# Kernel tuning notes

Hardware: AMD Instinct MI355X
Metric: run time of the kernel (lower is better)

The kernel has to match this reference:

```python
import jax, jax.numpy as jnp
import numpy as np

LN_EPS = 1e-5

def setup_inputs() -> dict:
    key = jax.random.key(0)
    k1, k2, k3 = jax.random.split(key, 3)
    L, B, D = 2048, 8, 1024
    x = jax.random.normal(k1, (L, B, D), dtype=jnp.float32)
    c = jnp.zeros((B, D), dtype=jnp.float32)
    W = jax.random.normal(k2, (D, 3 * D), dtype=jnp.float32) * 0.02
    # bias init from _init_bias: u-bias 0, f-bias 0.5, r-bias 0
    b = jnp.concatenate([jnp.zeros(D), jnp.full((D,), 0.5), jnp.zeros(D)]).astype(jnp.float32)
    gamma = jnp.ones((D,), dtype=jnp.float32)
    beta = jnp.zeros((D,), dtype=jnp.float32)
    return {"x": x, "c": c, "W": W, "b": b, "gamma": gamma, "beta": beta}

def reference(x, c, W, b, gamma, beta):
    # LayerNorm over last dim
    mu = jnp.mean(x, axis=-1, keepdims=True)
    var = jnp.mean(jnp.square(x - mu), axis=-1, keepdims=True)
    x_norm = (x - mu) * jax.lax.rsqrt(var + LN_EPS) * gamma + beta
    # Fused u/f/r projection: [L,B,3D]
    ufr = jnp.einsum('lbd,de->lbe', x_norm, W) + b
    u, f, r = jnp.split(ufr, 3, axis=-1)
    f_gate = jax.nn.sigmoid(f)
    r_gate = jax.nn.sigmoid(r)
    # Linear recurrence c_t = f_t * c_{t-1} + (1-f_t) * u_t via scan over time
    def step(c_prev, fu):
        f_t, u_t = fu
        c_t = f_t * c_prev + (1.0 - f_t) * u_t
        return c_t, c_t
    last_c, c_stack = jax.lax.scan(step, c, (f_gate, u))
    hs = r_gate * jnp.tanh(c_stack) + (1.0 - r_gate) * x_norm
    return x + hs, last_c
```

## Files before the change

### kernel.cpp

```cpp
#include <hip/hip_runtime.h>
#include <hip/hip_bf16.h>
#include <hip/hip_fp8.h>


typedef unsigned short u16;
typedef unsigned char u8;
typedef __bf16 bf16x8 __attribute__((ext_vector_type(8)));
typedef float f32x4 __attribute__((ext_vector_type(4)));

#define L_DIM 2048
#define B_DIM 8
#define D_DIM 1024
#define M_DIM (L_DIM * B_DIM)
#define K_DIM D_DIM
#define N_DIM (3 * D_DIM)
#define NCH 32
#define CLEN (L_DIM / NCH)
#define NT (K_DIM / 64)

#define LDS_B 65536
#define LDS_DUMMY 131072
#define LDS_TOTAL 147456
#define L8_B 32768
#define L8_DUMMY 65536
#define L8_TOTAL 73728

__device__ __forceinline__ float bf2f(u16 h) {
    unsigned int u = ((unsigned int)h) << 16;
    float f;
    __builtin_memcpy(&f, &u, 4);
    return f;
}

__device__ __forceinline__ u16 f2bf(float f) {
    unsigned int u;
    __builtin_memcpy(&u, &f, 4);
    u = u + 0x7fff + ((u >> 16) & 1);
    return (u16)(u >> 16);
}

__device__ __forceinline__ u8 f2e4(float v) {
    __hip_fp8_e4m3 t(v);
    return (u8)t.__x;
}

__device__ __forceinline__ void async16(void* lds, const void* g) {
    __builtin_amdgcn_global_load_lds(
        (const __attribute__((address_space(1))) void*)g,
        (__attribute__((address_space(3))) void*)lds, 16, 0, 0);
}

__global__ __launch_bounds__(256) void ln_kernel(const float* __restrict__ x,
                                                 const float* __restrict__ gamma,
                                                 const float* __restrict__ beta,
                                                 u16* __restrict__ xn,
                                                 u8* __restrict__ xq,
                                                 float2* __restrict__ mrs) {
    int row = blockIdx.x;
    int tid = threadIdx.x;
    const float4* xr = (const float4*)(x + (size_t)row * D_DIM);
    float4 v = xr[tid];
    float s = v.x + v.y + v.z + v.w;
    float q = v.x * v.x + v.y * v.y + v.z * v.z + v.w * v.w;
    #pragma unroll
    for (int off = 32; off; off >>= 1) {
        s += __shfl_down(s, off);
        q += __shfl_down(q, off);
    }
    __shared__ float ss[4], qq[4];
    int lane = tid & 63, wv = tid >> 6;
    if (lane == 0) { ss[wv] = s; qq[wv] = q; }
    __syncthreads();
    s = ss[0] + ss[1] + ss[2] + ss[3];
    q = qq[0] + qq[1] + qq[2] + qq[3];
    float mu = s * (1.0f / D_DIM);
    float var = q * (1.0f / D_DIM) - mu * mu;
    float rs = rsqrtf(var + 1e-5f);
    if (tid == 0) mrs[row] = make_float2(mu, rs);
    float4 g = ((const float4*)gamma)[tid];
    float4 bt = ((const float4*)beta)[tid];
    float n0 = (v.x - mu) * rs * g.x + bt.x;
    float n1 = (v.y - mu) * rs * g.y + bt.y;
    float n2 = (v.z - mu) * rs * g.z + bt.z;
    float n3 = (v.w - mu) * rs * g.w + bt.w;
    ushort4 o;
    o.x = f2bf(n0); o.y = f2bf(n1); o.z = f2bf(n2); o.w = f2bf(n3);
    ((ushort4*)(xn + (size_t)row * D_DIM))[tid] = o;
    uchar4 o8;
    o8.x = f2e4(n0); o8.y = f2e4(n1); o8.z = f2e4(n2); o8.w = f2e4(n3);
    ((uchar4*)(xq + (size_t)row * D_DIM))[tid] = o8;
}

__global__ __launch_bounds__(256) void wt_kernel(const float* __restrict__ W,
                                                 u16* __restrict__ Wt,
                                                 u8* __restrict__ Wf8) {
    __shared__ float t[64][65];
    int k0 = blockIdx.x * 64;
    int n0 = blockIdx.y * 64;
    int col = threadIdx.x & 63;
    int rg4 = threadIdx.x >> 6;
    #pragma unroll
    for (int j = 0; j < 16; ++j) {
        int r = rg4 * 16 + j;
        t[r][col] = W[(size_t)(k0 + r) * N_DIM + n0 + col];
    }
    __syncthreads();
    if (n0 < 1024) {
        #pragma unroll
        for (int j = 0; j < 16; ++j) {
            int nr = rg4 * 16 + j;
            Wt[(size_t)(n0 + nr) * K_DIM + k0 + col] = f2bf(t[col][nr]);
        }
    } else {
        #pragma unroll
        for (int j = 0; j < 16; ++j) {
            int nr = rg4 * 16 + j;
            Wf8[(size_t)(n0 - 1024 + nr) * K_DIM + k0 + col] = f2e4(t[col][nr] * 64.0f);
        }
    }
}

__global__ __launch_bounds__(512, 2) void gemm_kernel(const u16* __restrict__ A,
                                                      const u16* __restrict__ Bt,
                                                      const float* __restrict__ bias,
                                                      u16* __restrict__ uo) {
    extern __shared__ char lds[];
    const int tid = threadIdx.x;
    const int wave = tid >> 6, lane = tid & 63;
    const int lm = lane & 15, lg = lane >> 4;
    const int wm = wave >> 2, wn = wave & 3;
    const int m0 = blockIdx.x * 256;
    const int n0 = blockIdx.y * 256;

    const int xk0 = ((0 | lg) ^ (lm & 7)) << 4;
    const int xk1 = ((4 | lg) ^ (lm & 7)) << 4;
    const char* pA0 = lds + (wm * 128 + lm) * 128 + xk0;
    const char* pA1 = lds + (wm * 128 + lm) * 128 + xk1;
    const char* pB0 = lds + LDS_B + (wn * 64 + lm) * 128 + xk0;
    const char* pB1 = lds + LDS_B + (wn * 64 + lm) * 128 + xk1;

    const int c1 = 512 + tid;
    const int r0 = tid >> 3, cc0 = (tid & 7) ^ (r0 & 7);
    const int r1 = c1 >> 3, cc1 = (c1 & 7) ^ (r1 & 7);
    const char* gA0 = (const char*)A + ((size_t)(m0 + r0) * K_DIM + cc0 * 8) * 2;
    const char* gA1 = (const char*)A + ((size_t)(m0 + r1) * K_DIM + cc1 * 8) * 2;
    const char* gB0 = (const char*)Bt + ((size_t)(n0 + r0) * K_DIM + cc0 * 8) * 2;
    const char* gB1 = (const char*)Bt + ((size_t)(n0 + r1) * K_DIM + cc1 * 8) * 2;
    char* dstW = lds + wave * 1024;

    f32x4 acc[8][4] = {};
    bf16x8 av[4], aw[4], bv0[4], bv1[4];

    auto stageA = [&](int t1, int h) {
        char* dst = (t1 < NT) ? (dstW + ((t1 & 1) << 15) + (h << 14))
                              : (lds + LDS_DUMMY + wave * 1024);
        int ko = ((t1 & 15) << 7) + (h << 18);
        async16(dst,        gA0 + ko);
        async16(dst + 8192, gA1 + ko);
    };
    auto stageB = [&](int t2, int h) {
        char* dst = (t2 < NT) ? (dstW + LDS_B + ((t2 & 1) << 15) + (h << 14))
                              : (lds + LDS_DUMMY + wave * 1024);
        int ko = ((t2 & 15) << 7) + (h << 18);
        async16(dst,        gB0 + ko);
        async16(dst + 8192, gB1 + ko);
    };

#define LDA(dst, pbase, bb, mf0)                                                \
    do { _Pragma("unroll")                                                      \
        for (int q = 0; q < 4; ++q)                                             \
            dst[q] = *(const bf16x8*)(pbase + (bb) * 32768 + ((mf0) + q) * 2048); \
    } while (0)

#define LDB(dst, pbase, bb)                                                     \
    do { _Pragma("unroll")                                                      \
        for (int nf = 0; nf < 4; ++nf)                                          \
            dst[nf] = *(const bf16x8*)(pbase + (bb) * 32768 + nf * 2048);       \
    } while (0)

#define MFMA16(r0q, afr, bfr)                                                   \
    do { _Pragma("unroll")                                                      \
        for (int q = 0; q < 4; ++q)                                             \
            _Pragma("unroll")                                                   \
            for (int nf = 0; nf < 4; ++nf)                                      \
                acc[(r0q) + q][nf] = __builtin_amdgcn_mfma_f32_16x16x32_bf16(   \
                    afr[q], bfr[nf], acc[(r0q) + q][nf], 0, 0, 0);              \
    } while (0)

#define PH_SYNC()                                                               \
    do { __builtin_amdgcn_s_barrier();                                          \
         asm volatile("s_waitcnt lgkmcnt(0)");                                  \
         __builtin_amdgcn_sched_barrier(0); } while (0)

#define TILE_BODY(t, bb)                                                        \
    do {                                                                        \
        LDA(av, pA0, bb, 0);                                                    \
        LDB(bv0, pB0, bb);                                                      \
        stageA((t) + 1, 0);                                                     \
        PH_SYNC();                                                              \
        __builtin_amdgcn_s_setprio(1);  MFMA16(0, av, bv0);                     \
        __builtin_amdgcn_s_setprio(0);  __builtin_amdgcn_s_barrier();           \
        LDA(av, pA1, bb, 0);                                                    \
        LDB(bv1, pB1, bb);                                                      \
        stageA((t) + 1, 1);                                                     \
        PH_SYNC();                                                              \
        __builtin_amdgcn_s_setprio(1);  MFMA16(0, av, bv1);                     \
        __builtin_amdgcn_s_setprio(0);  __builtin_amdgcn_s_barrier();           \
        LDA(aw, pA0, bb, 4);                                                    \
        stageB((t) + 2, 0);                                                     \
        PH_SYNC();                                                              \
        __builtin_amdgcn_s_setprio(1);  MFMA16(4, aw, bv0);                     \
        __builtin_amdgcn_s_setprio(0);  __builtin_amdgcn_s_barrier();           \
        LDA(aw, pA1, bb, 4);                                                    \
        stageB((t) + 2, 1);                                                     \
        PH_SYNC();                                                              \
        __builtin_amdgcn_s_setprio(1);  MFMA16(4, aw, bv1);                     \
        __builtin_amdgcn_s_setprio(0);                                          \
        asm volatile("s_waitcnt vmcnt(4)" ::: "memory");                        \
        __builtin_amdgcn_s_barrier();                                           \
    } while (0)

    stageA(0, 0); stageA(0, 1);
    stageB(0, 0); stageB(0, 1);
    stageB(1, 0); stageB(1, 1);
    asm volatile("s_waitcnt vmcnt(4)" ::: "memory");
    __builtin_amdgcn_s_barrier();

    for (int t = 0; t < NT; t += 2) {
        TILE_BODY(t, 0);
        TILE_BODY(t + 1, 1);
    }

    float bb4[4];
    #pragma unroll
    for (int nf = 0; nf < 4; ++nf) bb4[nf] = bias[n0 + wn * 64 + nf * 16 + lm];
    const int cmb = n0 + wn * 64 + lm;
    #pragma unroll
    for (int mf = 0; mf < 8; ++mf) {
        #pragma unroll
        for (int j = 0; j < 4; ++j) {
            int row = m0 + wm * 128 + mf * 16 + lg * 4 + j;
            u16* rp = uo + (size_t)row * D_DIM + cmb;
            #pragma unroll
            for (int nf = 0; nf < 4; ++nf)
                rp[nf * 16] = f2bf(acc[mf][nf][j] + bb4[nf]);
        }
    }
#undef LDA
#undef LDB
#undef MFMA16
#undef PH_SYNC
#undef TILE_BODY
}

__global__ __launch_bounds__(512, 2) void gemm8_kernel(const u8* __restrict__ A8,
                                                       const u8* __restrict__ B8,
                                                       const float* __restrict__ bias,
                                                       u16* __restrict__ fo,
                                                       u16* __restrict__ ro) {
    extern __shared__ char lds[];
    const int tid = threadIdx.x;
    const int wave = tid >> 6, lane = tid & 63;
    const int lm = lane & 15, lg = lane >> 4;
    const int wm = wave >> 2, wn = wave & 3;
    const int m0 = blockIdx.x * 256;
    const int n0 = blockIdx.y * 256;

    const int sl = (lg & 1) * 8;
    const int xq0 = (((0 + (lg >> 1)) ^ (lm & 3)) << 4) + sl;
    const int xq1 = (((2 + (lg >> 1)) ^ (lm & 3)) << 4) + sl;
    const char* pA0 = lds + (wm * 128 + lm) * 64 + xq0;
    const char* pA1 = lds + (wm * 128 + lm) * 64 + xq1;
    const char* pB0 = lds + L8_B + (wn * 64 + lm) * 64 + xq0;
    const char* pB1 = lds + L8_B + (wn * 64 + lm) * 64 + xq1;

    const int r0 = tid >> 2, cq0 = (tid & 3) ^ (r0 & 3);
    const char* gA = (const char*)A8 + (size_t)(m0 + r0) * K_DIM + cq0 * 16;
    const char* gB = (const char*)B8 + (size_t)(n0 + r0) * K_DIM + cq0 * 16;
    char* dstW = lds + wave * 1024;

    f32x4 acc[8][4] = {};
    long av[4], aw[4], bv0[4], bv1[4];

    auto stageA = [&](int t1, int h) {
        char* dst = (t1 < NT) ? (dstW + ((t1 & 1) << 14) + (h << 13))
                              : (lds + L8_DUMMY + wave * 1024);
        async16(dst, gA + ((t1 & 15) << 6) + (h << 17));
    };
    auto stageB = [&](int t2, int h) {
        char* dst = (t2 < NT) ? (dstW + L8_B + ((t2 & 1) << 14) + (h << 13))
                              : (lds + L8_DUMMY + wave * 1024);
        async16(dst, gB + ((t2 & 15) << 6) + (h << 17));
    };

#define LDA8(dst, pbase, bb, mf0)                                               \
    do { _Pragma("unroll")                                                      \
        for (int q = 0; q < 4; ++q)                                             \
            dst[q] = *(const long*)(pbase + (bb) * 16384 + ((mf0) + q) * 1024); \
    } while (0)

#define LDB8(dst, pbase, bb)                                                    \
    do { _Pragma("unroll")                                                      \
        for (int nf = 0; nf < 4; ++nf)                                          \
            dst[nf] = *(const long*)(pbase + (bb) * 16384 + nf * 1024);         \
    } while (0)

#define MFMA16F8(r0q, afr, bfr)                                                 \
    do { _Pragma("unroll")                                                      \
        for (int q = 0; q < 4; ++q)                                             \
            _Pragma("unroll")                                                   \
            for (int nf = 0; nf < 4; ++nf)                                      \
                acc[(r0q) + q][nf] = __builtin_amdgcn_mfma_f32_16x16x32_fp8_fp8(\
                    afr[q], bfr[nf], acc[(r0q) + q][nf], 0, 0, 0);              \
    } while (0)

#define PH_SYNC()                                                               \
    do { __builtin_amdgcn_s_barrier();                                          \
         asm volatile("s_waitcnt lgkmcnt(0)");                                  \
         __builtin_amdgcn_sched_barrier(0); } while (0)

#define TILE_BODY8(t, bb)                                                       \
    do {                                                                        \
        LDA8(av, pA0, bb, 0);                                                   \
        LDB8(bv0, pB0, bb);                                                     \
        stageA((t) + 1, 0);                                                     \
        PH_SYNC();                                                              \
        __builtin_amdgcn_s_setprio(1);  MFMA16F8(0, av, bv0);                   \
        __builtin_amdgcn_s_setprio(0);  __builtin_amdgcn_s_barrier();           \
        LDA8(av, pA1, bb, 0);                                                   \
        LDB8(bv1, pB1, bb);                                                     \
        stageA((t) + 1, 1);                                                     \
        PH_SYNC();                                                              \
        __builtin_amdgcn_s_setprio(1);  MFMA16F8(0, av, bv1);                   \
        __builtin_amdgcn_s_setprio(0);  __builtin_amdgcn_s_barrier();           \
        LDA8(aw, pA0, bb, 4);                                                   \
        stageB((t) + 2, 0);                                                     \
        PH_SYNC();                                                              \
        __builtin_amdgcn_s_setprio(1);  MFMA16F8(4, aw, bv0);                   \
        __builtin_amdgcn_s_setprio(0);  __builtin_amdgcn_s_barrier();           \
        LDA8(aw, pA1, bb, 4);                                                   \
        stageB((t) + 2, 1);                                                     \
        PH_SYNC();                                                              \
        __builtin_amdgcn_s_setprio(1);  MFMA16F8(4, aw, bv1);                   \
        __builtin_amdgcn_s_setprio(0);                                          \
        asm volatile("s_waitcnt vmcnt(2)" ::: "memory");                        \
        __builtin_amdgcn_s_barrier();                                           \
    } while (0)

    stageA(0, 0); stageA(0, 1);
    stageB(0, 0); stageB(0, 1);
    stageB(1, 0); stageB(1, 1);
    asm volatile("s_waitcnt vmcnt(2)" ::: "memory");
    __builtin_amdgcn_s_barrier();

    for (int t = 0; t < NT; t += 2) {
        TILE_BODY8(t, 0);
        TILE_BODY8(t + 1, 1);
    }

    int seg = n0 >> 10;
    u16* outp = seg ? ro : fo;
    float bb4[4];
    #pragma unroll
    for (int nf = 0; nf < 4; ++nf) bb4[nf] = bias[1024 + n0 + wn * 64 + nf * 16 + lm];
    const int cmb = (n0 + wn * 64 + lm) & 1023;
    #pragma unroll
    for (int mf = 0; mf < 8; ++mf) {
        #pragma unroll
        for (int j = 0; j < 4; ++j) {
            int row = m0 + wm * 128 + mf * 16 + lg * 4 + j;
            u16* rp = outp + (size_t)row * D_DIM + cmb;
            #pragma unroll
            for (int nf = 0; nf < 4; ++nf) {
                float val = acc[mf][nf][j] * 0.015625f + bb4[nf];
                rp[nf * 16] = f2bf(1.0f / (1.0f + __expf(-val)));
            }
        }
    }
#undef LDA8
#undef LDB8
#undef MFMA16F8
#undef PH_SYNC
#undef TILE_BODY8
}

__global__ __launch_bounds__(256) void scan1_kernel(const u16* __restrict__ fg,
                                                    const u16* __restrict__ u,
                                                    float* __restrict__ Aa,
                                                    float* __restrict__ Ss) {
    int ch = blockIdx.x;
    int bd = (blockIdx.y * 256 + threadIdx.x) * 2;
    int b = bd >> 10, d = bd & 1023;
    float a0 = 1.0f, a1 = 1.0f, s0 = 0.0f, s1 = 0.0f;
    for (int t = ch * CLEN; t < ch * CLEN + CLEN; ++t) {
        size_t idx = ((size_t)(t * B_DIM + b) << 10) + d;
        ushort2 f2 = *(const ushort2*)(fg + idx);
        ushort2 u2 = *(const ushort2*)(u + idx);
        float f0 = bf2f(f2.x), f1 = bf2f(f2.y);
        float v0 = bf2f(u2.x), v1 = bf2f(u2.y);
        s0 = f0 * s0 + (1.0f - f0) * v0;
        s1 = f1 * s1 + (1.0f - f1) * v1;
        a0 *= f0;
        a1 *= f1;
    }
    int o = ch * 8192 + bd;
    *(float2*)(Aa + o) = make_float2(a0, a1);
    *(float2*)(Ss + o) = make_float2(s0, s1);
}

__global__ __launch_bounds__(256) void scan2_kernel(const float* __restrict__ Aa,
                                                    const float* __restrict__ Ss,
                                                    const float* __restrict__ c0,
                                                    float* __restrict__ cs,
                                                    float* __restrict__ lastc) {
    int bd = blockIdx.x * 256 + threadIdx.x;
    float c = c0[bd];
    #pragma unroll 4
    for (int ch = 0; ch < NCH; ++ch) {
        cs[ch * 8192 + bd] = c;
        c = Aa[ch * 8192 + bd] * c + Ss[ch * 8192 + bd];
    }
    lastc[bd] = c;
}

__global__ __launch_bounds__(256) void scan3_kernel(const float* __restrict__ cs,
                                                    const u16* __restrict__ fg,
                                                    const u16* __restrict__ u,
                                                    const u16* __restrict__ rg,
                                                    const float2* __restrict__ mrs,
                                                    const float* __restrict__ gamma,
                                                    const float* __restrict__ beta,
                                                    const float* __restrict__ x,
                                                    float* __restrict__ out) {
    int ch = blockIdx.x;
    int bd = (blockIdx.y * 256 + threadIdx.x) * 2;
    int b = bd >> 10, d = bd & 1023;
    float2 gm = *(const float2*)(gamma + d);
    float2 bt = *(const float2*)(beta + d);
    float c0v = cs[ch * 8192 + bd];
    float c1v = cs[ch * 8192 + bd + 1];
    for (int t = ch * CLEN; t < ch * CLEN + CLEN; ++t) {
        size_t idx = ((size_t)(t * B_DIM + b) << 10) + d;
        ushort2 f2 = *(const ushort2*)(fg + idx);
        ushort2 u2 = *(const ushort2*)(u + idx);
        ushort2 r2 = *(const ushort2*)(rg + idx);
        float2 x2 = *(const float2*)(x + idx);
        float2 mr = mrs[t * B_DIM + b];
        float f0 = bf2f(f2.x), f1 = bf2f(f2.y);
        float v0 = bf2f(u2.x), v1 = bf2f(u2.y);
        float r0 = bf2f(r2.x), r1 = bf2f(r2.y);
        float n0 = (x2.x - mr.x) * mr.y * gm.x + bt.x;
        float n1 = (x2.y - mr.x) * mr.y * gm.y + bt.y;
        c0v = f0 * c0v + (1.0f - f0) * v0;
        c1v = f1 * c1v + (1.0f - f1) * v1;
        float h0 = r0 * tanhf(c0v) + (1.0f - r0) * n0;
        float h1 = r1 * tanhf(c1v) + (1.0f - r1) * n1;
        *(float2*)(out + idx) = make_float2(x2.x + h0, x2.y + h1);
    }
}

extern "C" void kernel_launch(void* const* d_in, const int* in_sizes, int n_in,
                              void* d_out, int out_size, void* d_ws, size_t ws_size,
                              hipStream_t stream) {
    const float* x     = (const float*)d_in[0];
    const float* c0    = (const float*)d_in[1];
    const float* W     = (const float*)d_in[2];
    const float* b     = (const float*)d_in[3];
    const float* gamma = (const float*)d_in[4];
    const float* beta  = (const float*)d_in[5];
    float* out = (float*)d_out;
    float* lastc = out + (size_t)M_DIM * D_DIM;
    u8* xq = (u8*)d_out;

    char* w = (char*)d_ws;
    u16* xn = (u16*)w;  w += (size_t)M_DIM * D_DIM * 2;
    u16* Wt = (u16*)w;  w += (size_t)N_DIM * K_DIM * 2;
    u16* ug = (u16*)w;  w += (size_t)M_DIM * D_DIM * 2;
    u16* fg = (u16*)w;  w += (size_t)M_DIM * D_DIM * 2;
    u16* rg = (u16*)w;  w += (size_t)M_DIM * D_DIM * 2;
    float* Aa = (float*)w; w += (size_t)NCH * 8192 * 4;
    float* Ss = (float*)w; w += (size_t)NCH * 8192 * 4;
    float* cs = (float*)w; w += (size_t)NCH * 8192 * 4;
    float2* mrs = (float2*)w; w += (size_t)M_DIM * 8;
    u8* Wf8 = (u8*)w; w += (size_t)2048 * K_DIM;

    hipFuncSetAttribute(reinterpret_cast<const void*>(gemm_kernel),
                        hipFuncAttributeMaxDynamicSharedMemorySize, LDS_TOTAL);
    hipFuncSetAttribute(reinterpret_cast<const void*>(gemm8_kernel),
                        hipFuncAttributeMaxDynamicSharedMemorySize, L8_TOTAL);

    ln_kernel<<<M_DIM, 256, 0, stream>>>(x, gamma, beta, xn, xq, mrs);
    wt_kernel<<<dim3(K_DIM / 64, N_DIM / 64), 256, 0, stream>>>(W, Wt, Wf8);
    gemm_kernel<<<dim3(M_DIM / 256, 4), 512, LDS_TOTAL, stream>>>(xn, Wt, b, ug);
    gemm8_kernel<<<dim3(M_DIM / 256, 8), 512, L8_TOTAL, stream>>>(xq, Wf8, b, fg, rg);
    scan1_kernel<<<dim3(NCH, 16), 256, 0, stream>>>(fg, ug, Aa, Ss);
    scan2_kernel<<<32, 256, 0, stream>>>(Aa, Ss, c0, cs, lastc);
    scan3_kernel<<<dim3(NCH, 16), 256, 0, stream>>>(cs, fg, ug, rg, mrs, gamma, beta, x, out);
}
```

Measured before the change: 214.5 us.

## Double FP8 GEMM K-tile depth to 128 with wider LDS swizzle

The FP8 gate GEMM now stages 128-byte K slices per tile instead of 64, halving the number of main-loop iterations and barriers. The LDS layout grows to 128-byte rows with an 8-way XOR swizzle, and each thread issues two async 16-byte loads per stage. Wait counts and the four-phase tile body are adjusted so every A fragment is reused across more B fragments. LDS use rises from 72KB to 144KB, which likely drops occupancy from two blocks per CU to one.

```diff
diff --git a/kernel.cpp b/kernel.cpp
--- a/kernel.cpp
+++ b/kernel.cpp
@@ -17,13 +17,11 @@
 #define NCH 32
 #define CLEN (L_DIM / NCH)
 #define NT (K_DIM / 64)
+#define NT8 (K_DIM / 128)
 
 #define LDS_B 65536
 #define LDS_DUMMY 131072
 #define LDS_TOTAL 147456
-#define L8_B 32768
-#define L8_DUMMY 65536
-#define L8_TOTAL 73728
 
 __device__ __forceinline__ float bf2f(u16 h) {
     unsigned int u = ((unsigned int)h) << 16;
@@ -266,52 +264,60 @@
     const int m0 = blockIdx.x * 256;
     const int n0 = blockIdx.y * 256;
 
-    const int sl = (lg & 1) * 8;
-    const int xq0 = (((0 + (lg >> 1)) ^ (lm & 3)) << 4) + sl;
-    const int xq1 = (((2 + (lg >> 1)) ^ (lm & 3)) << 4) + sl;
-    const char* pA0 = lds + (wm * 128 + lm) * 64 + xq0;
-    const char* pA1 = lds + (wm * 128 + lm) * 64 + xq1;
-    const char* pB0 = lds + L8_B + (wn * 64 + lm) * 64 + xq0;
-    const char* pB1 = lds + L8_B + (wn * 64 + lm) * 64 + xq1;
-
-    const int r0 = tid >> 2, cq0 = (tid & 3) ^ (r0 & 3);
-    const char* gA = (const char*)A8 + (size_t)(m0 + r0) * K_DIM + cq0 * 16;
-    const char* gB = (const char*)B8 + (size_t)(n0 + r0) * K_DIM + cq0 * 16;
+    const int lgb = (lg & 1) * 8, lg2 = lg >> 1;
+    const int xq0 = (((0 + lg2) ^ (lm & 7)) << 4) + lgb;
+    const int xq1 = (((2 + lg2) ^ (lm & 7)) << 4) + lgb;
+    const int xq2 = (((4 + lg2) ^ (lm & 7)) << 4) + lgb;
+    const int xq3 = (((6 + lg2) ^ (lm & 7)) << 4) + lgb;
+    const char* pA = lds + (wm * 128 + lm) * 128;
+    const char* pB = lds + LDS_B + (wn * 64 + lm) * 128;
+
+    const int c1 = 512 + tid;
+    const int r0 = tid >> 3, cc0 = (tid & 7) ^ (r0 & 7);
+    const int r1 = c1 >> 3, cc1 = (c1 & 7) ^ (r1 & 7);
+    const char* gA0 = (const char*)A8 + (size_t)(m0 + r0) * K_DIM + cc0 * 16;
+    const char* gA1 = (const char*)A8 + (size_t)(m0 + r1) * K_DIM + cc1 * 16;
+    const char* gB0 = (const char*)B8 + (size_t)(n0 + r0) * K_DIM + cc0 * 16;
+    const char* gB1 = (const char*)B8 + (size_t)(n0 + r1) * K_DIM + cc1 * 16;
     char* dstW = lds + wave * 1024;
 
     f32x4 acc[8][4] = {};
-    long av[4], aw[4], bv0[4], bv1[4];
+    long av[8], bv0[4], bv1[4], bv2[4], bv3[4];
 
     auto stageA = [&](int t1, int h) {
-        char* dst = (t1 < NT) ? (dstW + ((t1 & 1) << 14) + (h << 13))
-                              : (lds + L8_DUMMY + wave * 1024);
-        async16(dst, gA + ((t1 & 15) << 6) + (h << 17));
+        char* dst = (t1 < NT8) ? (dstW + ((t1 & 1) << 15) + (h << 14))
+                               : (lds + LDS_DUMMY + wave * 1024);
+        int ko = ((t1 & 7) << 7) + (h << 17);
+        async16(dst,        gA0 + ko);
+        async16(dst + 8192, gA1 + ko);
     };
     auto stageB = [&](int t2, int h) {
-        char* dst = (t2 < NT) ? (dstW + L8_B + ((t2 & 1) << 14) + (h << 13))
-                              : (lds + L8_DUMMY + wave * 1024);
-        async16(dst, gB + ((t2 & 15) << 6) + (h << 17));
+        char* dst = (t2 < NT8) ? (dstW + LDS_B + ((t2 & 1) << 15) + (h << 14))
+                               : (lds + LDS_DUMMY + wave * 1024);
+        int ko = ((t2 & 7) << 7) + (h << 17);
+        async16(dst,        gB0 + ko);
+        async16(dst + 8192, gB1 + ko);
     };
 
-#define LDA8(dst, pbase, bb, mf0)                                               \
+#define LDA8(xq, bb)                                                            \
     do { _Pragma("unroll")                                                      \
-        for (int q = 0; q < 4; ++q)                                             \
-            dst[q] = *(const long*)(pbase + (bb) * 16384 + ((mf0) + q) * 1024); \
-    } while (0)
-
-#define LDB8(dst, pbase, bb)                                                    \
+        for (int q = 0; q < 8; ++q)                                             \
+            av[q] = *(const long*)(pA + (bb) * 32768 + q * 2048 + (xq));        \
+    } while (0)
+
+#define LDB8(dst, xq, bb)                                                       \
     do { _Pragma("unroll")                                                      \
         for (int nf = 0; nf < 4; ++nf)                                          \
-            dst[nf] = *(const long*)(pbase + (bb) * 16384 + nf * 1024);         \
-    } while (0)
-
-#define MFMA16F8(r0q, afr, bfr)                                                 \
+            dst[nf] = *(const long*)(pB + (bb) * 32768 + nf * 2048 + (xq));     \
+    } while (0)
+
+#define MFMA32F8(bfr)                                                           \
     do { _Pragma("unroll")                                                      \
-        for (int q = 0; q < 4; ++q)                                             \
+        for (int q = 0; q < 8; ++q)                                             \
             _Pragma("unroll")                                                   \
             for (int nf = 0; nf < 4; ++nf)                                      \
-                acc[(r0q) + q][nf] = __builtin_amdgcn_mfma_f32_16x16x32_fp8_fp8(\
-                    afr[q], bfr[nf], acc[(r0q) + q][nf], 0, 0, 0);              \
+                acc[q][nf] = __builtin_amdgcn_mfma_f32_16x16x32_fp8_fp8(        \
+                    av[q], bfr[nf], acc[q][nf], 0, 0, 0);                       \
     } while (0)
 
 #define PH_SYNC()                                                               \
@@ -321,39 +327,41 @@
 
 #define TILE_BODY8(t, bb)                                                       \
     do {                                                                        \
-        LDA8(av, pA0, bb, 0);                                                   \
-        LDB8(bv0, pB0, bb);                                                     \
+        LDA8(xq0, bb);                                                          \
+        LDB8(bv0, xq0, bb);                                                     \
+        LDB8(bv1, xq1, bb);                                                     \
         stageA((t) + 1, 0);                                                     \
         PH_SYNC();                                                              \
-        __builtin_amdgcn_s_setprio(1);  MFMA16F8(0, av, bv0);                   \
+        __builtin_amdgcn_s_setprio(1);  MFMA32F8(bv0);                          \
         __builtin_amdgcn_s_setprio(0);  __builtin_amdgcn_s_barrier();           \
-        LDA8(av, pA1, bb, 0);                                                   \
-        LDB8(bv1, pB1, bb);                                                     \
+        LDA8(xq1, bb);                                                          \
+        LDB8(bv2, xq2, bb);                                                     \
+        LDB8(bv3, xq3, bb);                                                     \
         stageA((t) + 1, 1);                                                     \
         PH_SYNC();                                                              \
-        __builtin_amdgcn_s_setprio(1);  MFMA16F8(0, av, bv1);                   \
+        __builtin_amdgcn_s_setprio(1);  MFMA32F8(bv1);                          \
         __builtin_amdgcn_s_setprio(0);  __builtin_amdgcn_s_barrier();           \
-        LDA8(aw, pA0, bb, 4);                                                   \
+        LDA8(xq2, bb);                                                          \
         stageB((t) + 2, 0);                                                     \
         PH_SYNC();                                                              \
-        __builtin_amdgcn_s_setprio(1);  MFMA16F8(4, aw, bv0);                   \
+        __builtin_amdgcn_s_setprio(1);  MFMA32F8(bv2);                          \
         __builtin_amdgcn_s_setprio(0);  __builtin_amdgcn_s_barrier();           \
-        LDA8(aw, pA1, bb, 4);                                                   \
+        LDA8(xq3, bb);                                                          \
         stageB((t) + 2, 1);                                                     \
         PH_SYNC();                                                              \
-        __builtin_amdgcn_s_setprio(1);  MFMA16F8(4, aw, bv1);                   \
+        __builtin_amdgcn_s_setprio(1);  MFMA32F8(bv3);                          \
         __builtin_amdgcn_s_setprio(0);                                          \
-        asm volatile("s_waitcnt vmcnt(2)" ::: "memory");                        \
+        asm volatile("s_waitcnt vmcnt(4)" ::: "memory");                        \
         __builtin_amdgcn_s_barrier();                                           \
     } while (0)
 
     stageA(0, 0); stageA(0, 1);
     stageB(0, 0); stageB(0, 1);
     stageB(1, 0); stageB(1, 1);
-    asm volatile("s_waitcnt vmcnt(2)" ::: "memory");
+    asm volatile("s_waitcnt vmcnt(4)" ::: "memory");
     __builtin_amdgcn_s_barrier();
 
-    for (int t = 0; t < NT; t += 2) {
+    for (int t = 0; t < NT8; t += 2) {
         TILE_BODY8(t, 0);
         TILE_BODY8(t + 1, 1);
     }
@@ -379,7 +387,7 @@
     }
 #undef LDA8
 #undef LDB8
-#undef MFMA16F8
+#undef MFMA32F8
 #undef PH_SYNC
 #undef TILE_BODY8
 }
@@ -487,12 +495,12 @@
     hipFuncSetAttribute(reinterpret_cast<const void*>(gemm_kernel),
                         hipFuncAttributeMaxDynamicSharedMemorySize, LDS_TOTAL);
     hipFuncSetAttribute(reinterpret_cast<const void*>(gemm8_kernel),
-                        hipFuncAttributeMaxDynamicSharedMemorySize, L8_TOTAL);
+                        hipFuncAttributeMaxDynamicSharedMemorySize, LDS_TOTAL);
 
     ln_kernel<<<M_DIM, 256, 0, stream>>>(x, gamma, beta, xn, xq, mrs);
     wt_kernel<<<dim3(K_DIM / 64, N_DIM / 64), 256, 0, stream>>>(W, Wt, Wf8);
     gemm_kernel<<<dim3(M_DIM / 256, 4), 512, LDS_TOTAL, stream>>>(xn, Wt, b, ug);
-    gemm8_kernel<<<dim3(M_DIM / 256, 8), 512, L8_TOTAL, stream>>>(xq, Wf8, b, fg, rg);
+    gemm8_kernel<<<dim3(M_DIM / 256, 8), 512, LDS_TOTAL, stream>>>(xq, Wf8, b, fg, rg);
     scan1_kernel<<<dim3(NCH, 16), 256, 0, stream>>>(fg, ug, Aa, Ss);
     scan2_kernel<<<32, 256, 0, stream>>>(Aa, Ss, c0, cs, lastc);
     scan3_kernel<<<dim3(NCH, 16), 256, 0, stream>>>(cs, fg, ug, rg, mrs, gamma, beta, x, out);
```

Result: faster. 204.8 us (-4.5%).
